# Performance work log

Hardware: AMD Instinct MI355X
Metric: run time of the kernel (lower is better)

## Reference

```python
import math
import jax
import jax.numpy as jnp
import numpy as np

B, N, NPOINT, K = 8, 2048, 512, 16
CIN = 64
MLP = [64, 128, 256]
M_W = 8    # PAConv weight-bank size
HID = 16   # scorenet hidden width
GEOM = 10  # 3 rel-xyz + 1 dist + 3 norm + 3 angles


def setup_inputs():
    key = jax.random.key(0)
    ks = jax.random.split(key, 40)
    inp = {}
    inp['xyz'] = jax.random.normal(ks[0], (B, 3, N), jnp.float32)
    inp['norm'] = jax.random.normal(ks[1], (B, 3, N), jnp.float32)
    inp['X_axis'] = jax.random.normal(ks[2], (B, 3, N), jnp.float32)
    inp['Y_axis'] = jax.random.normal(ks[3], (B, 3, N), jnp.float32)
    inp['points'] = jax.random.normal(ks[4], (B, CIN, N), jnp.float32) * 0.5
    cin = CIN
    ki = 5
    for l, cout in enumerate(MLP):
        inp['w1_%d' % l] = jax.random.normal(ks[ki], (HID, GEOM), jnp.float32) / np.sqrt(GEOM); ki += 1
        inp['b1_%d' % l] = jnp.zeros((HID,), jnp.float32)
        inp['w2_%d' % l] = jax.random.normal(ks[ki], (M_W, HID), jnp.float32) / np.sqrt(HID); ki += 1
        inp['b2_%d' % l] = jnp.zeros((M_W,), jnp.float32)
        inp['bank_%d' % l] = jax.random.normal(ks[ki], (M_W, cin, cout), jnp.float32) / np.sqrt(cin); ki += 1
        if l < len(MLP) - 1:
            inp['gamma_%d' % l] = jnp.ones((cout,), jnp.float32)
            inp['beta_%d' % l] = jnp.zeros((cout,), jnp.float32)
        cin = cout
    return inp


def _group(t, idx):
    # t: (B, C, N), idx: (B, ...) int -> (B, C, ...)
    return jax.vmap(lambda p, i: p[:, i])(t, idx)


def _fps(xyz_t, npoint):
    # xyz_t: (B, N, 3) -> (B, npoint) int32; standard iterative FPS starting at index 0
    b, n, _ = xyz_t.shape
    def body(i, c):
        idxs, dists, far = c
        idxs = idxs.at[:, i].set(far)
        centroid = jnp.take_along_axis(xyz_t, far[:, None, None], axis=1)  # (B,1,3)
        d = jnp.sum((xyz_t - centroid) ** 2, axis=-1)
        dists = jnp.minimum(dists, d)
        return idxs, dists, jnp.argmax(dists, axis=-1).astype(jnp.int32)
    idxs = jnp.zeros((b, npoint), jnp.int32)
    dists = jnp.full((b, n), 1e10, xyz_t.dtype)
    far = jnp.zeros((b,), jnp.int32)
    idxs, _, _ = jax.lax.fori_loop(0, npoint, body, (idxs, dists, far))
    return idxs


def _sqdist(a, b):
    # a: (B, P, 3), b: (B, N, 3) -> (B, P, N)
    return (jnp.sum(a ** 2, -1)[:, :, None] + jnp.sum(b ** 2, -1)[:, None, :]
            - 2.0 * jnp.einsum('bpc,bnc->bpn', a, b))


def _angles(gxyz, gn, gX, gY):
    # all (B, 3, P, K) -> (B, 3, P, K); normalized angles to z(norm)/x/y frame axes
    nn = jnp.linalg.norm(gxyz, axis=1)
    def ang(v):
        c = jnp.sum(gxyz * v, axis=1) / (nn * jnp.linalg.norm(v, axis=1) + 1e-8)
        return jnp.arccos(jnp.clip(c, -1.0, 1.0)) / math.pi
    return jnp.stack([ang(gn), ang(gX), ang(gY)], axis=1)


def _paconv(geom, feats, w1, b1, w2, b2, bank, gamma=None, beta=None, act=True):
    # ScoreNet over geometric channels -> softmax scores over M weight matrices
    h = jax.nn.relu(jnp.einsum('hg,bgpk->bhpk', w1, geom) + b1[None, :, None, None])
    s = jax.nn.softmax(jnp.einsum('mh,bhpk->bmpk', w2, h) + b2[None, :, None, None], axis=1)
    out = jnp.einsum('bcpk,mco,bmpk->bopk', feats, bank, s)
    if gamma is not None:
        mu = out.mean(axis=(0, 2, 3), keepdims=True)
        var = out.var(axis=(0, 2, 3), keepdims=True)
        out = (out - mu) / jnp.sqrt(var + 1e-5) * gamma[None, :, None, None] + beta[None, :, None, None]
    return jax.nn.relu(out) if act else out


def reference(xyz, norm, X_axis, Y_axis, points,
              w1_0, b1_0, w2_0, b2_0, bank_0, gamma_0, beta_0,
              w1_1, b1_1, w2_1, b2_1, bank_1, gamma_1, beta_1,
              w1_2, b1_2, w2_2, b2_2, bank_2):
    xyz_t = jnp.transpose(xyz, (0, 2, 1))           # (B,N,3)
    fidx = _fps(xyz_t, NPOINT)                      # (B,NPOINT)
    new_xyz = _group(xyz, fidx)                     # (B,3,NPOINT)
    sq = _sqdist(jnp.transpose(new_xyz, (0, 2, 1)), xyz_t)  # (B,NPOINT,N)
    idx = jax.lax.top_k(-sq, K)[1]                  # (B,NPOINT,K) ascending distance
    grouped_xyz = _group(xyz, idx) - new_xyz[:, :, :, None]  # (B,3,NPOINT,K)
    dist = jnp.sqrt(jnp.sum(grouped_xyz ** 2, axis=1) + 1e-10)  # (B,NPOINT,K)
    dmin = dist.min(axis=2, keepdims=True)
    dist = (dist - dmin) / (dist.max(axis=2, keepdims=True) - dmin + 1e-10)
    new_points = _group(points, idx)                # (B,CIN,NPOINT,K)
    grouped_norm = _group(norm, idx)
    grouped_X = _group(X_axis, idx)
    grouped_Y = _group(Y_axis, idx)
    grouped_angles = _angles(grouped_xyz, grouped_norm, grouped_X, grouped_Y)
    new_norm = grouped_norm[:, :, :, 0]
    new_X = grouped_X[:, :, :, 0]
    new_Y = grouped_Y[:, :, :, 0]
    geom = jnp.concatenate([grouped_xyz, dist[:, None], grouped_norm, grouped_angles], axis=1)  # (B,10,NPOINT,K)
    new_points = _paconv(geom, new_points, w1_0, b1_0, w2_0, b2_0, bank_0, gamma_0, beta_0, act=True)
    new_points = _paconv(geom, new_points, w1_1, b1_1, w2_1, b2_1, bank_1, gamma_1, beta_1, act=True)
    new_points = _paconv(geom, new_points, w1_2, b1_2, w2_2, b2_2, bank_2, None, None, act=False)
    new_points = jnp.max(new_points, axis=3)        # (B,MLP[-1],NPOINT)
    return (new_xyz, new_norm, new_X, new_Y, new_points)
```

## Files before the change

kernel.cpp:

```cpp
#include <hip/hip_runtime.h>
#include <math.h>

#define NBATCH 8
#define NPTS   2048
#define NPOINT 512
#define KNB    16
#define NROWS  (NBATCH*NPOINT*KNB)

#define TRANS_BASE  NBATCH
#define ZERO_BID    (NBATCH + 256)
#define CONV_BASE   (NBATCH + 257)
#define KNN_BASE    (NBATCH + 257 + 1408)
#define MEGA_GRID   (KNN_BASE + 1024)

typedef unsigned short ushort_t;
typedef unsigned int   uint_t;
typedef unsigned long long ull_t;
typedef __attribute__((ext_vector_type(8))) short  short8;
typedef __attribute__((ext_vector_type(4))) float  f32x4;
typedef __attribute__((ext_vector_type(2))) float  f32x2;

#define B0_OFF 0
#define B1_OFF 32768
#define B2_OFF 98304
#define BT_TOT 360448

#define LDS_BARRIER() asm volatile("s_waitcnt lgkmcnt(0)\n\ts_barrier" ::: "memory")

__device__ __align__(16) int      g_fidx [NBATCH * NPOINT];
__device__ __align__(16) int      g_fready[NBATCH * NPOINT];
__device__ __align__(16) int      g_knn [NROWS];
__device__ __align__(16) float    g_sums[1024];
__device__ __align__(16) float    g_pT  [NBATCH * NPTS * 64];
__device__ __align__(16) float    g_S   [(size_t)3 * NROWS * 8];
__device__ __align__(16) float    g_act1[(size_t)NROWS * 64];
__device__ __align__(16) float    g_act2[(size_t)NROWS * 128];
__device__ __align__(16) ushort_t g_bankF[BT_TOT];

__device__ __forceinline__ ushort_t f2bf(float f) {
    uint_t u = __float_as_uint(f);
    return (ushort_t)((u + 0x7FFFu + ((u >> 16) & 1u)) >> 16);
}

template<int CTRL>
__device__ __forceinline__ ull_t dpp_u64(ull_t k) {
    int lo = (int)(uint_t)k;
    int hi = (int)(uint_t)(k >> 32);
    int slo = __builtin_amdgcn_update_dpp(0, lo, CTRL, 0xF, 0xF, true);
    int shi = __builtin_amdgcn_update_dpp(0, hi, CTRL, 0xF, 0xF, true);
    return ((ull_t)(uint_t)shi << 32) | (uint_t)slo;
}

__device__ __forceinline__ ull_t dpp_max_u64(ull_t key) {
    { ull_t s = dpp_u64<0x111>(key); if (s > key) key = s; }
    { ull_t s = dpp_u64<0x112>(key); if (s > key) key = s; }
    { ull_t s = dpp_u64<0x114>(key); if (s > key) key = s; }
    { ull_t s = dpp_u64<0x118>(key); if (s > key) key = s; }
    { ull_t s = dpp_u64<0x142>(key); if (s > key) key = s; }
    { ull_t s = dpp_u64<0x143>(key); if (s > key) key = s; }
    return key;
}

template<int CTRL>
__device__ __forceinline__ uint_t dpp_u32(uint_t v) {
    return (uint_t)__builtin_amdgcn_update_dpp(0, (int)v, CTRL, 0xF, 0xF, true);
}

__device__ __forceinline__ uint_t dpp_max_u32(uint_t v) {
    { uint_t s = dpp_u32<0x111>(v); if (s > v) v = s; }
    { uint_t s = dpp_u32<0x112>(v); if (s > v) v = s; }
    { uint_t s = dpp_u32<0x114>(v); if (s > v) v = s; }
    { uint_t s = dpp_u32<0x118>(v); if (s > v) v = s; }
    { uint_t s = dpp_u32<0x142>(v); if (s > v) v = s; }
    { uint_t s = dpp_u32<0x143>(v); if (s > v) v = s; }
    return v;
}

template<int COUT>
__device__ __forceinline__ void bank_frag(const float* __restrict__ bank,
                                          ushort_t* __restrict__ dst, int e) {
    const int j = e & 7;
    const int lane = (e >> 3) & 63;
    const int rem = e >> 9;
    constexpr int NTL = COUT / 16;
    const int nt = rem % NTL;
    const int kc = rem / NTL;
    const int q = lane >> 4, nlo = lane & 15;
    const int k = kc * 32 + q * 8 + j;
    const int n = nt * 16 + nlo;
    dst[e] = f2bf(bank[(size_t)k * COUT + n]);
}

__global__ __launch_bounds__(256, 5) void mega_kernel(
    const float* __restrict__ xyz, const float* __restrict__ points,
    const float* __restrict__ bank0, const float* __restrict__ bank1,
    const float* __restrict__ bank2,
    const float* __restrict__ nrm, const float* __restrict__ Xa,
    const float* __restrict__ Ya,
    const float* __restrict__ w1_0, const float* __restrict__ b1_0,
    const float* __restrict__ w2_0, const float* __restrict__ b2_0,
    const float* __restrict__ w1_1, const float* __restrict__ b1_1,
    const float* __restrict__ w2_1, const float* __restrict__ b2_1,
    const float* __restrict__ w1_2, const float* __restrict__ b1_2,
    const float* __restrict__ w2_2, const float* __restrict__ b2_2) {
    __shared__ float smem[3 * NPTS];
    __shared__ ull_t s_key[2][4];
    const int bid = blockIdx.x;
    const int t = threadIdx.x;

    if (bid >= NBATCH) {
        if (bid < ZERO_BID) {
            float (*tile)[65] = reinterpret_cast<float(*)[65]>(smem);
            const int blk = bid - TRANS_BASE;
            const int b = blk >> 5;
            const int n0 = (blk & 31) * 64;
            const int lane = t & 63, q = t >> 6;
            #pragma unroll
            for (int i = 0; i < 16; ++i) {
                int c = q * 16 + i;
                tile[c][lane] = points[(b * 64 + c) * NPTS + n0 + lane];
            }
            __syncthreads();
            #pragma unroll
            for (int i = 0; i < 16; ++i) {
                int n = q * 16 + i;
                g_pT[(size_t)(b * NPTS + n0 + n) * 64 + lane] = tile[lane][n];
            }
            return;
        } else if (bid == ZERO_BID) {
            g_sums[t] = 0.0f;
            g_sums[256 + t] = 0.0f;
            g_sums[512 + t] = 0.0f;
            g_sums[768 + t] = 0.0f;
            return;
        } else if (bid < KNN_BASE) {
            const int e = (bid - CONV_BASE) * 256 + t;
            if (e < 32768) {
                bank_frag<64>(bank0, g_bankF + B0_OFF, e);
            } else if (e < 98304) {
                bank_frag<128>(bank1, g_bankF + B1_OFF, e - 32768);
            } else {
                bank_frag<256>(bank2, g_bankF + B2_OFF, e - 98304);
            }
            return;
        }

        {
            const float* w1p[3] = {w1_0, w1_1, w1_2};
            const float* b1p[3] = {b1_0, b1_1, b1_2};
            const float* w2p[3] = {w2_0, w2_1, w2_2};
            const float* b2p[3] = {b2_0, b2_1, b2_2};
            #pragma unroll
            for (int l = 0; l < 3; ++l) {
                if (t < 160) smem[l * 160 + t] = w1p[l][t];
                if (t < 16)  smem[480 + l * 16 + t] = b1p[l][t];
                if (t < 128) smem[528 + l * 128 + t] = w2p[l][t];
                if (t < 8)   smem[912 + l * 8 + t] = b2p[l][t];
            }
        }
        __syncthreads();

        const int wave = (bid - KNN_BASE) * 4 + (t >> 6);
        const int lane = t & 63;
        const int b = wave >> 9;
        const float* xb = xyz + b * 3 * NPTS;

        int fv = __hip_atomic_load(&g_fready[wave], __ATOMIC_RELAXED,
                                   __HIP_MEMORY_SCOPE_AGENT);
        while (fv == 0) {
            __builtin_amdgcn_s_sleep(8);
            fv = __hip_atomic_load(&g_fready[wave], __ATOMIC_RELAXED,
                                   __HIP_MEMORY_SCOPE_AGENT);
        }
        if (lane == 0)
            __hip_atomic_store(&g_fready[wave], 0, __ATOMIC_RELAXED,
                               __HIP_MEMORY_SCOPE_AGENT);
        const int fi = (fv - 1) & (NPTS - 1);
        int nmine = 0;

        {
            #pragma clang fp contract(off)
            float ax = xb[fi];
            float ay = xb[NPTS + fi];
            float az = xb[2*NPTS + fi];
            float sa = ax*ax + ay*ay; sa = sa + az*az;
            float d[32];
            #pragma unroll
            for (int j = 0; j < 32; ++j) {
                int pp = j * 64 + lane;
                float bx = xb[pp];
                float by = xb[NPTS + pp];
                float bz = xb[2*NPTS + pp];
                float sb = bx*bx + by*by; sb = sb + bz*bz;
                float dot = ax*bx + ay*by; dot = dot + az*bz;
                float t1 = sa + sb;
                float t2 = 2.0f * dot;
                d[j] = t1 - t2;
            }
            for (int r = 0; r < KNB; ++r) {
                float best = 1e30f; int bi = 0x7fffffff;
                #pragma unroll
                for (int j = 0; j < 32; ++j) {
                    if (d[j] < best) { best = d[j]; bi = j * 64 + lane; }
                }
                uint_t ub = __float_as_uint(best);
                ub = (ub & 0x80000000u) ? ~ub : (ub | 0x80000000u);
                ull_t key = ((ull_t)(~ub) << 32) | (uint_t)(~bi);
                key = dpp_max_u64(key);
                uint_t wlo = (uint_t)__builtin_amdgcn_readlane((int)(uint_t)key, 63);
                bi = (int)(~wlo) & (NPTS - 1);
                if (lane == 0) g_knn[wave * KNB + r] = bi;
                if (lane == r) nmine = bi;
                int rl = bi & 63, rs = bi >> 6;
                if (lane == rl) {
                    #pragma unroll
                    for (int j = 0; j < 32; ++j) if (j == rs) d[j] = 1e30f;
                }
            }
        }

        if (lane < 16) {
            const int row = wave * KNB + lane;
            const int n = nmine & (NPTS - 1);
            const float* nb = nrm + b * 3 * NPTS;
            const float* Xb = Xa  + b * 3 * NPTS;
            const float* Yb = Ya  + b * 3 * NPTS;
            float gx, gy, gz, sq, draw, nnv;
            {
                #pragma clang fp contract(off)
                gx = xb[n]        - xb[fi];
                gy = xb[NPTS + n] - xb[NPTS + fi];
                gz = xb[2*NPTS+n] - xb[2*NPTS+fi];
                sq = gx*gx + gy*gy;
                sq = sq + gz*gz;
                draw = sqrtf(sq + 1e-10f);
                nnv = sqrtf(sq);
            }
            float dmin = draw, dmax = draw;
            #pragma unroll
            for (int m = 1; m < 16; m <<= 1) {
                dmin = fminf(dmin, __shfl_xor(dmin, m, 16));
                dmax = fmaxf(dmax, __shfl_xor(dmax, m, 16));
            }
            float dist;
            {
                #pragma clang fp contract(off)
                dist = (draw - dmin) / ((dmax - dmin) + 1e-10f);
            }
            float nx = nb[n], ny = nb[NPTS+n], nz = nb[2*NPTS+n];
            float Xx = Xb[n], Xy = Xb[NPTS+n], Xz = Xb[2*NPTS+n];
            float Yx = Yb[n], Yy = Yb[NPTS+n], Yz = Yb[2*NPTS+n];
            float g[10];
            g[0]=gx; g[1]=gy; g[2]=gz; g[3]=dist; g[4]=nx; g[5]=ny; g[6]=nz;
            {
                float vs[3][3] = {{nx,ny,nz},{Xx,Xy,Xz},{Yx,Yy,Yz}};
                #pragma unroll
                for (int a = 0; a < 3; ++a) {
                    float vx=vs[a][0], vy=vs[a][1], vz=vs[a][2];
                    float dot, nv;
                    {
                        #pragma clang fp contract(off)
                        dot = gx*vx + gy*vy; dot = dot + gz*vz;
                        float s2 = vx*vx + vy*vy; s2 = s2 + vz*vz;
                        nv = sqrtf(s2);
                    }
                    float cc = dot / (nnv * nv + 1e-8f);
                    cc = fminf(1.0f, fmaxf(-1.0f, cc));
                    g[7+a] = acosf(cc) / 3.14159274101257324f;
                }
            }
            #pragma unroll
            for (int l = 0; l < 3; ++l) {
                float h[16];
                #pragma unroll
                for (int i = 0; i < 16; ++i) {
                    float a = smem[480 + l * 16 + i];
                    #pragma unroll
                    for (int j = 0; j < 10; ++j) a += smem[l * 160 + i * 10 + j] * g[j];
                    h[i] = fmaxf(a, 0.0f);
                }
                float e[8]; float mx = -1e30f;
                #pragma unroll
                for (int m = 0; m < 8; ++m) {
                    float a = smem[912 + l * 8 + m];
                    #pragma unroll
                    for (int j = 0; j < 16; ++j) a += smem[528 + l * 128 + m * 16 + j] * h[j];
                    e[m] = a; mx = fmaxf(mx, a);
                }
                float sum = 0.0f;
                #pragma unroll
                for (int m = 0; m < 8; ++m) { e[m] = expf(e[m] - mx); sum += e[m]; }
                #pragma unroll
                for (int m = 0; m < 8; ++m)
                    g_S[(size_t)l * NROWS * 8 + (size_t)row * 8 + m] = e[m] / sum;
            }
        }
        return;
    }

    {
        #pragma clang fp contract(off)
        const int b = bid;
        const int lane = t & 63, w = t >> 6;
        const float* xb = xyz + b * 3 * NPTS;
        float* s_x = smem;
        float* s_y = smem + NPTS;
        float* s_z = smem + 2 * NPTS;
        f32x2 xp[4], yp[4], zp[4];
        float d[8];
        {
            const float4* xq = reinterpret_cast<const float4*>(xb + t * 8);
            const float4* yq = reinterpret_cast<const float4*>(xb + NPTS + t * 8);
            const float4* zq = reinterpret_cast<const float4*>(xb + 2 * NPTS + t * 8);
            float4 a0 = xq[0], a1 = xq[1];
            float4 b0 = yq[0], b1 = yq[1];
            float4 c0 = zq[0], c1 = zq[1];
            xp[0] = (f32x2){a0.x, a0.y}; xp[1] = (f32x2){a0.z, a0.w};
            xp[2] = (f32x2){a1.x, a1.y}; xp[3] = (f32x2){a1.z, a1.w};
            yp[0] = (f32x2){b0.x, b0.y}; yp[1] = (f32x2){b0.z, b0.w};
            yp[2] = (f32x2){b1.x, b1.y}; yp[3] = (f32x2){b1.z, b1.w};
            zp[0] = (f32x2){c0.x, c0.y}; zp[1] = (f32x2){c0.z, c0.w};
            zp[2] = (f32x2){c1.x, c1.y}; zp[3] = (f32x2){c1.z, c1.w};
            *reinterpret_cast<float4*>(s_x + t * 8)     = a0;
            *reinterpret_cast<float4*>(s_x + t * 8 + 4) = a1;
            *reinterpret_cast<float4*>(s_y + t * 8)     = b0;
            *reinterpret_cast<float4*>(s_y + t * 8 + 4) = b1;
            *reinterpret_cast<float4*>(s_z + t * 8)     = c0;
            *reinterpret_cast<float4*>(s_z + t * 8 + 4) = c1;
            #pragma unroll
            for (int j = 0; j < 8; ++j) d[j] = 1e10f;
        }
        __syncthreads();
        int far = 0;
        for (int i = 0; i < NPOINT; ++i) {
            if (t == 0) {
                g_fidx[b * NPOINT + i] = far;
                __hip_atomic_store(&g_fready[b * NPOINT + i], far + 1,
                                   __ATOMIC_RELAXED, __HIP_MEMORY_SCOPE_AGENT);
            }
            const float cx = s_x[far], cy = s_y[far], cz = s_z[far];
            const f32x2 cxp = (f32x2){cx, cx};
            const f32x2 cyp = (f32x2){cy, cy};
            const f32x2 czp = (f32x2){cz, cz};
            uint_t bb = 0u;
            #pragma unroll
            for (int a = 0; a < 4; ++a) {
                f32x2 dx = xp[a] - cxp;
                f32x2 dy = yp[a] - cyp;
                f32x2 dz = zp[a] - czp;
                f32x2 s2 = dx*dx + dy*dy;
                s2 = s2 + dz*dz;
                float dn0 = fminf(d[2*a],   s2[0]);
                float dn1 = fminf(d[2*a+1], s2[1]);
                d[2*a] = dn0; d[2*a+1] = dn1;
                uint_t u0 = __float_as_uint(dn0);
                uint_t u1 = __float_as_uint(dn1);
                bb = (u0 > bb) ? u0 : bb;
                bb = (u1 > bb) ? u1 : bb;
            }
            uint_t wm = dpp_max_u32(bb);
            const uint_t wbits = (uint_t)__builtin_amdgcn_readlane((int)wm, 63);
            int li = 8;
            #pragma unroll
            for (int j = 7; j >= 0; --j)
                li = (__float_as_uint(d[j]) == wbits) ? j : li;
            ull_t mk = __ballot(li < 8);
            const int fl = __ffsll((unsigned long long)mk) - 1;
            const int wj = __builtin_amdgcn_readlane(li, fl);
            const int wp = (((w << 6) + fl) << 3) + wj;
            if (lane == 0) s_key[i & 1][w] = ((ull_t)wbits << 32) | (uint_t)(~wp);
            LDS_BARRIER();
            const ull_t* kb = s_key[i & 1];
            ull_t k0 = kb[0], k1 = kb[1], k2 = kb[2], k3 = kb[3];
            if (k1 > k0) k0 = k1;
            if (k3 > k2) k2 = k3;
            if (k2 > k0) k0 = k2;
            far = (int)(~(uint_t)k0) & (NPTS - 1);
        }
    }
}

template<int LAYER, int CIN, int COUT>
__global__ __launch_bounds__(256) void gemm_kernel(const float* __restrict__ gamma,
                                                   const float* __restrict__ beta,
                                                   float* __restrict__ dout,
                                                   const float* __restrict__ xyz,
                                                   const float* __restrict__ nrm,
                                                   const float* __restrict__ Xa,
                                                   const float* __restrict__ Ya) {
    if constexpr (LAYER == 0) {
        if (blockIdx.x >= 1024) {
            const int g = (blockIdx.x - 1024) * 256 + threadIdx.x;
            const int b = g / NPOINT, p = g % NPOINT;
            const int fi = g_fidx[g] & (NPTS - 1);
            const int n0 = g_knn[g * KNB] & (NPTS - 1);
            #pragma unroll
            for (int a = 0; a < 3; ++a) {
                dout[            (b*3 + a) * NPOINT + p] = xyz[(b*3 + a) * NPTS + fi];
                dout[12288 +     (b*3 + a) * NPOINT + p] = nrm[(b*3 + a) * NPTS + n0];
                dout[24576 +     (b*3 + a) * NPOINT + p] = Xa [(b*3 + a) * NPTS + n0];
                dout[36864 +     (b*3 + a) * NPOINT + p] = Ya [(b*3 + a) * NPTS + n0];
            }
            return;
        }
    }

    const float* __restrict__ A = (LAYER == 0) ? g_pT : (LAYER == 1) ? g_act1 : g_act2;
    float* __restrict__ O = (LAYER == 0) ? g_act1 : (LAYER == 1) ? g_act2 : dout;
    constexpr int NTT = COUT / 16;
    constexpr int NTW = NTT / 4;
    constexpr int CCM = CIN / 32;
    constexpr int BOFF = (LAYER == 0) ? B0_OFF : (LAYER == 1) ? B1_OFF : B2_OFF;
    __shared__ ushort_t As[2][64][36];
    __shared__ float s_scale[(LAYER >= 1) ? CIN : 1];
    __shared__ float s_shift[(LAYER >= 1) ? CIN : 1];
    __shared__ float s_rs[(LAYER < 2) ? COUT : 1];
    __shared__ float s_rss[(LAYER < 2) ? COUT : 1];

    const int t = threadIdx.x;
    const int lane = t & 63, w = t >> 6;
    const int q = lane >> 4, nlo = lane & 15;
    const int row0 = blockIdx.x * 64;
    const int arow_i = t >> 2, acg = t & 3;

    if constexpr (LAYER >= 1) {
        const float* sb = (LAYER == 1) ? g_sums : (g_sums + 256);
        if (t < CIN) {
            float mu  = sb[t] * (1.0f / 65536.0f);
            float var = sb[CIN + t] * (1.0f / 65536.0f) - mu * mu;
            var = fmaxf(var, 0.0f);
            float sc = gamma[t] / sqrtf(var + 1e-5f);
            s_scale[t] = sc;
            s_shift[t] = beta[t] - mu * sc;
        }
        __syncthreads();
    }

    size_t arow;
    if (LAYER == 0) {
        const int row = row0 + arow_i;
        const int b = row >> 13;
        const int n = g_knn[row] & (NPTS - 1);
        arow = (size_t)(b * NPTS + n) * 64;
    } else {
        arow = (size_t)(row0 + arow_i) * CIN;
    }
    const float* Sbase = g_S + (size_t)LAYER * NROWS * 8 + (size_t)(row0 + arow_i) * 8;

    float svv[8];
    #pragma unroll
    for (int m = 0; m < 8; ++m) svv[m] = Sbase[m];

    f32x4 acc[4][NTW];
    #pragma unroll
    for (int mi = 0; mi < 4; ++mi)
        #pragma unroll
        for (int ni = 0; ni < NTW; ++ni) acc[mi][ni] = (f32x4){0.f, 0.f, 0.f, 0.f};

    const ushort_t* fbase = g_bankF + BOFF + lane * 8;

    union FragU { uint4 u4; uint2 u2[2]; short8 s; };
    FragU B[2][NTW];
    #pragma unroll
    for (int ni = 0; ni < NTW; ++ni)
        B[0][ni].u4 = *reinterpret_cast<const uint4*>(fbase + (size_t)(w * NTW + ni) * 512);

    float vraw[8], vnext[8];
    {
        const float* ap = A + arow + acg * 8;
        float4 fa = *reinterpret_cast<const float4*>(ap);
        float4 fb = *reinterpret_cast<const float4*>(ap + 4);
        vraw[0]=fa.x; vraw[1]=fa.y; vraw[2]=fa.z; vraw[3]=fa.w;
        vraw[4]=fb.x; vraw[5]=fb.y; vraw[6]=fb.z; vraw[7]=fb.w;
    }

    int par = 0;
    for (int cc = 0; cc < CCM; ++cc) {
        float v[8];
        #pragma unroll
        for (int j = 0; j < 8; ++j) {
            if constexpr (LAYER >= 1) {
                const int c = cc * 32 + acg * 8 + j;
                v[j] = fmaxf(vraw[j] * s_scale[c] + s_shift[c], 0.f);
            } else {
                v[j] = vraw[j];
            }
        }
        #pragma unroll
        for (int m = 0; m < 8; ++m) {
            {
                const float sv = svv[m];
                uint_t* dst = reinterpret_cast<uint_t*>(&As[par][arow_i][acg * 8]);
                #pragma unroll
                for (int j = 0; j < 8; j += 2)
                    dst[j >> 1] = (uint_t)f2bf(sv * v[j]) | ((uint_t)f2bf(sv * v[j+1]) << 16);
            }
            if (m == 0) {
                const int ccn = (cc + 1 < CCM) ? cc + 1 : cc;
                const float* ap = A + arow + ccn * 32 + acg * 8;
                float4 fa = *reinterpret_cast<const float4*>(ap);
                float4 fb = *reinterpret_cast<const float4*>(ap + 4);
                vnext[0]=fa.x; vnext[1]=fa.y; vnext[2]=fa.z; vnext[3]=fa.w;
                vnext[4]=fb.x; vnext[5]=fb.y; vnext[6]=fb.z; vnext[7]=fb.w;
            }
            {
                const int kcn = (m < 7) ? ((m + 1) * CCM + cc)
                                        : ((cc + 1 < CCM) ? (cc + 1) : 0);
                #pragma unroll
                for (int ni = 0; ni < NTW; ++ni)
                    B[(m + 1) & 1][ni].u4 = *reinterpret_cast<const uint4*>(
                        fbase + (size_t)(kcn * NTT + w * NTW + ni) * 512);
            }
            LDS_BARRIER();
            FragU af[4];
            #pragma unroll
            for (int mi = 0; mi < 4; ++mi) {
                af[mi].u2[0] = *reinterpret_cast<const uint2*>(&As[par][mi*16 + nlo][q*8]);
                af[mi].u2[1] = *reinterpret_cast<const uint2*>(&As[par][mi*16 + nlo][q*8 + 4]);
            }
            #pragma unroll
            for (int ni = 0; ni < NTW; ++ni)
                #pragma unroll
                for (int mi = 0; mi < 4; ++mi)
                    acc[mi][ni] = __builtin_amdgcn_mfma_f32_16x16x32_bf16(
                        af[mi].s, B[m & 1][ni].s, acc[mi][ni], 0, 0, 0);
            par ^= 1;
        }
        #pragma unroll
        for (int j = 0; j < 8; ++j) vraw[j] = vnext[j];
    }

    if constexpr (LAYER == 2) {
        const int bp0 = row0 >> 4;
        #pragma unroll
        for (int mi = 0; mi < 4; ++mi) {
            const int bp = bp0 + mi;
            const int b = bp >> 9, p = bp & 511;
            #pragma unroll
            for (int ni = 0; ni < NTW; ++ni) {
                float mv = fmaxf(fmaxf(acc[mi][ni][0], acc[mi][ni][1]),
                                 fmaxf(acc[mi][ni][2], acc[mi][ni][3]));
                mv = fmaxf(mv, __shfl_xor(mv, 16));
                mv = fmaxf(mv, __shfl_xor(mv, 32));
                if (lane < 16) {
                    const int col = w * 64 + ni * 16 + nlo;
                    O[(size_t)(b * 256 + col) * NPOINT + p] = mv;
                }
            }
        }
    } else {
        #pragma unroll
        for (int mi = 0; mi < 4; ++mi)
            #pragma unroll
            for (int ni = 0; ni < NTW; ++ni)
                #pragma unroll
                for (int r2 = 0; r2 < 4; ++r2)
                    O[(size_t)(row0 + mi*16 + q*4 + r2) * COUT + w*NTW*16 + ni*16 + nlo] = acc[mi][ni][r2];
        #pragma unroll
        for (int ni = 0; ni < NTW; ++ni) {
            float s = 0.f, ss = 0.f;
            #pragma unroll
            for (int mi = 0; mi < 4; ++mi) {
                #pragma unroll
                for (int r2 = 0; r2 < 4; ++r2) {
                    float x = acc[mi][ni][r2];
                    s += x; ss += x * x;
                }
            }
            s  += __shfl_xor(s, 16);  s  += __shfl_xor(s, 32);
            ss += __shfl_xor(ss, 16); ss += __shfl_xor(ss, 32);
            if (q == 0) {
                const int c = w * NTW * 16 + ni * 16 + nlo;
                s_rs[c] = s;
                s_rss[c] = ss;
            }
        }
        __syncthreads();
        if (t < COUT) {
            float* sb = (LAYER == 0) ? g_sums : (g_sums + 256);
            atomicAdd(&sb[t], s_rs[t]);
            atomicAdd(&sb[COUT + t], s_rss[t]);
        }
    }
}

extern "C" void kernel_launch(void* const* d_in, const int* in_sizes, int n_in,
                              void* d_out, int out_size, void* d_ws, size_t ws_size,
                              hipStream_t stream) {
    const float* xyz    = (const float*)d_in[0];
    const float* nrm    = (const float*)d_in[1];
    const float* Xa     = (const float*)d_in[2];
    const float* Ya     = (const float*)d_in[3];
    const float* points = (const float*)d_in[4];
    const float* w1_0 = (const float*)d_in[5];  const float* b1_0 = (const float*)d_in[6];
    const float* w2_0 = (const float*)d_in[7];  const float* b2_0 = (const float*)d_in[8];
    const float* bank0 = (const float*)d_in[9];
    const float* g0 = (const float*)d_in[10];   const float* be0 = (const float*)d_in[11];
    const float* w1_1 = (const float*)d_in[12]; const float* b1_1 = (const float*)d_in[13];
    const float* w2_1 = (const float*)d_in[14]; const float* b2_1 = (const float*)d_in[15];
    const float* bank1 = (const float*)d_in[16];
    const float* g1 = (const float*)d_in[17];   const float* be1 = (const float*)d_in[18];
    const float* w1_2 = (const float*)d_in[19]; const float* b1_2 = (const float*)d_in[20];
    const float* w2_2 = (const float*)d_in[21]; const float* b2_2 = (const float*)d_in[22];
    const float* bank2 = (const float*)d_in[23];
    float* out = (float*)d_out;
    (void)d_ws; (void)ws_size; (void)in_sizes; (void)n_in; (void)out_size;

    mega_kernel<<<MEGA_GRID, 256, 0, stream>>>(xyz, points, bank0, bank1, bank2,
                                               nrm, Xa, Ya,
                                               w1_0, b1_0, w2_0, b2_0,
                                               w1_1, b1_1, w2_1, b2_1,
                                               w1_2, b1_2, w2_2, b2_2);
    gemm_kernel<0, 64, 64><<<1040, 256, 0, stream>>>(nullptr, nullptr, out, xyz, nrm, Xa, Ya);
    gemm_kernel<1, 64, 128><<<1024, 256, 0, stream>>>(g0, be0, nullptr, nullptr, nullptr, nullptr, nullptr);
    gemm_kernel<2, 128, 256><<<1024, 256, 0, stream>>>(g1, be1, out + 49152, nullptr, nullptr, nullptr, nullptr);
}
```

Measured before the change: 443.7 us.

## Use hardware packed bf16 convert, halve bank-prep blocks, prioritize FPS waves

Replaces the software round-to-nearest bf16 conversion with the v_cvt_pk_bf16_f32 instruction, both in the GEMM A-tile staging loop and in the bank-fragment prep. The prep now has each thread convert two elements, which halves the number of conversion blocks and shifts KNN_BASE down to match. It also raises the FPS wave priority with s_setprio and lengthens the sleep in the KNN spin-wait, so the FPS producer gets more issue slots while consumers poll less often. Rounding of NaN or edge cases may differ slightly from the software conversion.

```diff
diff --git a/kernel.cpp b/kernel.cpp
--- a/kernel.cpp
+++ b/kernel.cpp
@@ -10,7 +10,7 @@
 #define TRANS_BASE  NBATCH
 #define ZERO_BID    (NBATCH + 256)
 #define CONV_BASE   (NBATCH + 257)
-#define KNN_BASE    (NBATCH + 257 + 1408)
+#define KNN_BASE    (NBATCH + 257 + 704)
 #define MEGA_GRID   (KNN_BASE + 1024)
 
 typedef unsigned short ushort_t;
@@ -42,6 +42,12 @@
     return (ushort_t)((u + 0x7FFFu + ((u >> 16) & 1u)) >> 16);
 }
 
+__device__ __forceinline__ uint_t cvt_pk_bf16(float a, float b) {
+    uint_t r;
+    asm("v_cvt_pk_bf16_f32 %0, %1, %2" : "=v"(r) : "v"(a), "v"(b));
+    return r;
+}
+
 template<int CTRL>
 __device__ __forceinline__ ull_t dpp_u64(ull_t k) {
     int lo = (int)(uint_t)k;
@@ -77,18 +83,20 @@
 }
 
 template<int COUT>
-__device__ __forceinline__ void bank_frag(const float* __restrict__ bank,
-                                          ushort_t* __restrict__ dst, int e) {
-    const int j = e & 7;
-    const int lane = (e >> 3) & 63;
-    const int rem = e >> 9;
+__device__ __forceinline__ void bank_frag2(const float* __restrict__ bank,
+                                           uint_t* __restrict__ dst, int le) {
+    const int j = le & 7;
+    const int lane = (le >> 3) & 63;
+    const int rem = le >> 9;
     constexpr int NTL = COUT / 16;
     const int nt = rem % NTL;
     const int kc = rem / NTL;
     const int q = lane >> 4, nlo = lane & 15;
     const int k = kc * 32 + q * 8 + j;
     const int n = nt * 16 + nlo;
-    dst[e] = f2bf(bank[(size_t)k * COUT + n]);
+    const float f0 = bank[(size_t)k * COUT + n];
+    const float f1 = bank[(size_t)(k + 1) * COUT + n];
+    dst[le >> 1] = cvt_pk_bf16(f0, f1);
 }
 
 __global__ __launch_bounds__(256, 5) void mega_kernel(
@@ -134,13 +142,13 @@
             g_sums[768 + t] = 0.0f;
             return;
         } else if (bid < KNN_BASE) {
-            const int e = (bid - CONV_BASE) * 256 + t;
-            if (e < 32768) {
-                bank_frag<64>(bank0, g_bankF + B0_OFF, e);
-            } else if (e < 98304) {
-                bank_frag<128>(bank1, g_bankF + B1_OFF, e - 32768);
+            const int le = ((bid - CONV_BASE) * 256 + t) << 1;
+            if (le < 32768) {
+                bank_frag2<64>(bank0, reinterpret_cast<uint_t*>(g_bankF + B0_OFF), le);
+            } else if (le < 98304) {
+                bank_frag2<128>(bank1, reinterpret_cast<uint_t*>(g_bankF + B1_OFF), le - 32768);
             } else {
-                bank_frag<256>(bank2, g_bankF + B2_OFF, e - 98304);
+                bank_frag2<256>(bank2, reinterpret_cast<uint_t*>(g_bankF + B2_OFF), le - 98304);
             }
             return;
         }
@@ -168,7 +176,7 @@
         int fv = __hip_atomic_load(&g_fready[wave], __ATOMIC_RELAXED,
                                    __HIP_MEMORY_SCOPE_AGENT);
         while (fv == 0) {
-            __builtin_amdgcn_s_sleep(8);
+            __builtin_amdgcn_s_sleep(15);
             fv = __hip_atomic_load(&g_fready[wave], __ATOMIC_RELAXED,
                                    __HIP_MEMORY_SCOPE_AGENT);
         }
@@ -331,6 +339,7 @@
             for (int j = 0; j < 8; ++j) d[j] = 1e10f;
         }
         __syncthreads();
+        __builtin_amdgcn_s_setprio(2);
         int far = 0;
         for (int i = 0; i < NPOINT; ++i) {
             if (t == 0) {
@@ -493,7 +502,7 @@
                 uint_t* dst = reinterpret_cast<uint_t*>(&As[par][arow_i][acg * 8]);
                 #pragma unroll
                 for (int j = 0; j < 8; j += 2)
-                    dst[j >> 1] = (uint_t)f2bf(sv * v[j]) | ((uint_t)f2bf(sv * v[j+1]) << 16);
+                    dst[j >> 1] = cvt_pk_bf16(sv * v[j], sv * v[j + 1]);
             }
             if (m == 0) {
                 const int ccn = (cc + 1 < CCM) ? cc + 1 : cc;
```

Result: slower. 459.3 us (+3.5%).
